# Optimization experiments

Measured on AMD Instinct MI355X. Metric: run time of the kernel, lower is better.

The kernel has to match this reference:

```python
import jax, jax.numpy as jnp
import numpy as np

B, K, V = 8192, 1024, 2


def setup_inputs() -> dict:
    key = jax.random.key(0)
    k1, k2, k3, k4, k5, k6 = jax.random.split(key, 6)
    z = jax.random.normal(k1, (B, K), dtype=jnp.float32)
    # -1 means no intervention for that sample
    intervention_target = jax.random.randint(k2, (B,), -1, K)
    intervention_variant = jax.random.randint(k3, (B,), 0, V)
    raw_adjacency = jax.random.normal(k4, (K, K), dtype=jnp.float32) * 0.05
    intervention_means = jax.random.normal(k5, (K, V), dtype=jnp.float32)
    intervention_log_scales = jax.random.normal(k6, (K, V), dtype=jnp.float32) * 0.1
    return {
        "z": z,
        "intervention_target": intervention_target,
        "intervention_variant": intervention_variant,
        "raw_adjacency": raw_adjacency,
        "intervention_means": intervention_means,
        "intervention_log_scales": intervention_log_scales,
    }


def _scm_forward(z, target, variant, raw_adjacency, means, log_scales):
    Kd = z.shape[1]
    # strictly-lower-triangular adjacency (row j holds parents of node j)
    A = raw_adjacency * jnp.tril(jnp.ones((Kd, Kd), z.dtype), k=-1)

    def step(u, xs):
        a_row, mean_row, logsc_row, z_j, j = xs
        # forward substitution: u_j = z_j + sum_{i<j} A[j,i] * u_i
        # columns >= j of u are still zero and A row is zero there too
        value = z_j + u @ a_row  # [B]
        # intervention overwrite for samples with target == j
        m = mean_row[variant]                 # [B]
        s = jnp.exp(logsc_row[variant])       # [B]
        value = jnp.where(target == j, m + s * z_j, value)
        u = jax.lax.dynamic_update_slice(u, value[:, None], (0, j))
        return u, None

    u0 = jnp.zeros_like(z)
    xs = (A, means, log_scales, z.T, jnp.arange(Kd))
    u, _ = jax.lax.scan(step, u0, xs)
    return u


def reference(z, intervention_target, intervention_variant, raw_adjacency,
              intervention_means, intervention_log_scales):
    return _scm_forward(z, intervention_target, intervention_variant,
                        raw_adjacency, intervention_means, intervention_log_scales)
```

## Files before the change

### kernel.cpp

```cpp
#include <hip/hip_runtime.h>
#include <hip/hip_bf16.h>
#include <cstdint>

#define KDIM 1024
#define BDIM 8192
#define VDIM 2
#define NBLK 16

#if defined(__has_builtin)
#if __has_builtin(__builtin_amdgcn_global_load_lds)
#define HAS_GLL 1
#endif
#endif
#ifndef HAS_GLL
#define HAS_GLL 0
#endif

typedef __attribute__((ext_vector_type(8))) short short8;
typedef __attribute__((ext_vector_type(4))) float f32x4;

__device__ inline unsigned short f2bf(float x) {
  unsigned u = __builtin_bit_cast(unsigned, x);
  u = (u + 0x7FFFu + ((u >> 16) & 1u)) >> 16;
  return (unsigned short)u;
}

__device__ inline float bf2f(unsigned short x) {
  return __builtin_bit_cast(float, (unsigned)x << 16);
}


#define STAGE_T(DST, SRC, ROW0, COL0, LD)                                   \
  {                                                                         \
    const float* _s = (SRC);                                                \
    _Pragma("unroll") for (int _p = 0; _p < 4; ++_p) {                      \
      const int _m = _p * 16 + rw;                                          \
      float4 _v = *(const float4*)(_s + (size_t)((ROW0) + _m) * (LD) +      \
                                   (COL0) + 4 * k4);                        \
      (DST)[4 * k4 + 0][_m] = _v.x;                                         \
      (DST)[4 * k4 + 1][_m] = _v.y;                                         \
      (DST)[4 * k4 + 2][_m] = _v.z;                                         \
      (DST)[4 * k4 + 3][_m] = _v.w;                                         \
    }                                                                       \
  }

#define STAGE_D(DST, SRC, ROW0, COL0, LD)                                   \
  {                                                                         \
    const float* _s = (SRC);                                                \
    _Pragma("unroll") for (int _p = 0; _p < 4; ++_p) {                      \
      const int _kk = _p * 16 + rw;                                         \
      *(float4*)&(DST)[_kk][4 * k4] =                                       \
          *(const float4*)(_s + (size_t)((ROW0) + _kk) * (LD) + (COL0) +    \
                           4 * k4);                                         \
    }                                                                       \
  }

#define ZERO_ACC                                                            \
  _Pragma("unroll") for (int _a = 0; _a < 4; ++_a)                          \
      _Pragma("unroll") for (int _b = 0; _b < 4; ++_b) acc[_a][_b] = 0.f;

__device__ __forceinline__ void mac64(const float (*Ls)[68],
                                      const float (*Rs)[68], int tm, int tn,
                                      float acc[4][4]) {
#pragma unroll 4
  for (int k = 0; k < 64; ++k) {
    const float4 av = *(const float4*)&Ls[k][4 * tm];
    const float4 bv = *(const float4*)&Rs[k][4 * tn];
    const float aa[4] = {av.x, av.y, av.z, av.w};
    const float bb4[4] = {bv.x, bv.y, bv.z, bv.w};
#pragma unroll
    for (int a = 0; a < 4; ++a)
#pragma unroll
      for (int b = 0; b < 4; ++b) acc[a][b] += aa[a] * bb4[b];
  }
}

#define STORE_MT(R0, C0)                                                    \
  _Pragma("unroll") for (int _a = 0; _a < 4; ++_a) {                        \
    *(float4*)(MT + (size_t)((R0) + 4 * tm + _a) * KDIM + (C0) + 4 * tn) =  \
        make_float4(acc[_a][0], acc[_a][1], acc[_a][2], acc[_a][3]);        \
  }

#define MBF_TILE(R0, C0, BUF)                                               \
  {                                                                         \
    __syncthreads();                                                        \
    _Pragma("unroll") for (int _a = 0; _a < 4; ++_a)                        \
        _Pragma("unroll") for (int _b = 0; _b < 4; ++_b)                    \
            (BUF)[4 * tm + _a][4 * tn + _b] = acc[_a][_b];                  \
    __syncthreads();                                                        \
    const int _tr = tid >> 4, _tc = tid & 15;                               \
    _Pragma("unroll") for (int _p = 0; _p < 4; ++_p) {                      \
      const int _il = _p * 16 + _tr;                                        \
      ushort4 _o;                                                           \
      _o.x = f2bf((BUF)[4 * _tc + 0][_il]);                                 \
      _o.y = f2bf((BUF)[4 * _tc + 1][_il]);                                 \
      _o.z = f2bf((BUF)[4 * _tc + 2][_il]);                                 \
      _o.w = f2bf((BUF)[4 * _tc + 3][_il]);                                 \
      *(ushort4*)(Mbf + (size_t)((C0) + _il) * KDIM + (R0) + 4 * _tc) = _o; \
    }                                                                       \
  }

__global__ __launch_bounds__(256) void comb01(const float* __restrict__ A,
                                              float* __restrict__ MT,
                                              unsigned short* __restrict__ Mbf) {
  int b = blockIdx.x;
  const int rt = b & 1;
  const int jt = (b >> 1) & 1;
  const int s = b >> 2;
  const int base = s * 256;

  __shared__ float shpool[6 * 64 * 68];
  float (*Ls)[68] = (float(*)[68])(shpool);
  float (*Rs)[68] = (float(*)[68])(shpool + 4352);
  float (*tQ0L)[68] = (float(*)[68])(shpool + 2 * 4352);
  float (*tQ0H)[68] = (float(*)[68])(shpool + 3 * 4352);
  float (*tP0)[68] = (float(*)[68])(shpool + 4 * 4352);
  float (*tP1)[68] = (float(*)[68])(shpool + 5 * 4352);

  const int tid = threadIdx.x;
  const int k4 = tid & 15;
  const int rw = tid >> 4;
  const int tm = tid >> 4;
  const int tn = tid & 15;
  float acc[4][4];

  {
    float* Tt = shpool;
    float* As4 = shpool + 2 * 4352;
    const int g = tid >> 6;
    const int l = tid & 63;
    const int dbase = base + g * 64;
    float* Asg = As4 + g * 4160;

    for (int r = 0; r < 64; ++r)
      Asg[r * 65 + l] = A[(size_t)(dbase + r) * KDIM + dbase + l];
    __syncthreads();

    {
      const int h = l >> 5, c = l & 31;
      const float* Ah = Asg + (32 * h) * 65 + 32 * h;
      float m[32];
#pragma unroll
      for (int r = 0; r < 32; ++r) m[r] = (r == c) ? 1.f : 0.f;
#pragma unroll
      for (int r = 1; r < 32; ++r) {
        float a0 = 0.f, a1 = 0.f;
#pragma unroll
        for (int i = 0; i < 32; ++i) {
          if (i >= r) break;
          if (i & 1) a1 += Ah[r * 65 + i] * m[i];
          else       a0 += Ah[r * 65 + i] * m[i];
        }
        const float v = a0 + a1;
        m[r] = (r > c) ? v : m[r];
      }
      float* Th = Tt + g * 2112 + h * 1056;
#pragma unroll
      for (int r = 0; r < 32; ++r) Th[r * 33 + c] = m[r];
    }
    __syncthreads();

    const int tm8 = l >> 3, tn8 = l & 7;
    {
      float u[4][4];
#pragma unroll
      for (int a = 0; a < 4; ++a)
#pragma unroll
        for (int b2 = 0; b2 < 4; ++b2) u[a][b2] = 0.f;
      const float* T1 = Tt + g * 2112;
#pragma unroll
      for (int ki = 0; ki < 8; ++ki) {
        float4 av[4], bv[4];
#pragma unroll
        for (int a = 0; a < 4; ++a)
          av[a] = *(const float4*)&Asg[(32 + 4 * tm8 + a) * 65 + 4 * ki];
#pragma unroll
        for (int j = 0; j < 4; ++j)
          bv[j] = *(const float4*)&T1[(4 * ki + j) * 33 + 4 * tn8];
#pragma unroll
        for (int a = 0; a < 4; ++a) {
          const float aa[4] = {av[a].x, av[a].y, av[a].z, av[a].w};
#pragma unroll
          for (int j = 0; j < 4; ++j) {
            const float bb[4] = {bv[j].x, bv[j].y, bv[j].z, bv[j].w};
#pragma unroll
            for (int b2 = 0; b2 < 4; ++b2) u[a][b2] += aa[j] * bb[b2];
          }
        }
      }
#pragma unroll
      for (int a = 0; a < 4; ++a)
#pragma unroll
        for (int b2 = 0; b2 < 4; ++b2)
          Asg[(4 * tm8 + a) * 32 + 4 * tn8 + b2] = u[a][b2];
    }
    __syncthreads();

    {
      float t21[4][4];
#pragma unroll
      for (int a = 0; a < 4; ++a)
#pragma unroll
        for (int b2 = 0; b2 < 4; ++b2) t21[a][b2] = 0.f;
      const float* T2 = Tt + g * 2112 + 1056;
#pragma unroll
      for (int ki = 0; ki < 8; ++ki) {
        float4 av[4], bv[4];
#pragma unroll
        for (int a = 0; a < 4; ++a)
          av[a] = *(const float4*)&T2[(4 * tm8 + a) * 33 + 4 * ki];
#pragma unroll
        for (int j = 0; j < 4; ++j)
          bv[j] = *(const float4*)&Asg[(4 * ki + j) * 32 + 4 * tn8];
#pragma unroll
        for (int a = 0; a < 4; ++a) {
          const float aa[4] = {av[a].x, av[a].y, av[a].z, av[a].w};
#pragma unroll
          for (int j = 0; j < 4; ++j) {
            const float bb[4] = {bv[j].x, bv[j].y, bv[j].z, bv[j].w};
#pragma unroll
            for (int b2 = 0; b2 < 4; ++b2) t21[a][b2] += aa[j] * bb[b2];
          }
        }
      }
#pragma unroll
      for (int a = 0; a < 4; ++a)
#pragma unroll
        for (int b2 = 0; b2 < 4; ++b2)
          Asg[1024 + (4 * tm8 + a) * 32 + 4 * tn8 + b2] = t21[a][b2];
    }
    __syncthreads();

    {
      const float* T21 = Asg + 1024;
      const float* Tg = Tt + g * 2112;
      for (int r4 = 0; r4 < 16; ++r4) {
        float vals[4];
#pragma unroll
        for (int j = 0; j < 4; ++j) {
          const int r = 4 * r4 + j;
          float v;
          if (r < 32)
            v = (l < 32) ? Tg[r * 33 + l] : 0.f;
          else
            v = (l < 32) ? T21[(r - 32) * 32 + l]
                         : Tg[1056 + (r - 32) * 33 + (l - 32)];
          vals[j] = v;
        }
        *(float4*)(MT + (size_t)(dbase + l) * KDIM + dbase + 4 * r4) =
            make_float4(vals[0], vals[1], vals[2], vals[3]);
      }
      if (jt == 0 && rt == 0) {
        for (int r = 0; r < 64; ++r) {
          float v;
          if (r < 32)
            v = (l < 32) ? Tg[r * 33 + l] : 0.f;
          else
            v = (l < 32) ? T21[(r - 32) * 32 + l]
                         : Tg[1056 + (r - 32) * 33 + (l - 32)];
          Mbf[(size_t)(dbase + r) * KDIM + dbase + l] = f2bf(v);
        }
      }
    }
    __syncthreads();
  }

  if (jt == 0) {
    STAGE_T(Ls, MT, base, base, KDIM);
    STAGE_T(Rs, A, base + 64, base, KDIM);
    __syncthreads();
    ZERO_ACC;
    mac64(Ls, Rs, tm, tn, acc);
    __syncthreads();
#pragma unroll
    for (int a = 0; a < 4; ++a)
#pragma unroll
      for (int b2 = 0; b2 < 4; ++b2) tP0[4 * tn + b2][4 * tm + a] = acc[a][b2];
    STAGE_D(Rs, MT, base + 64, base + 64, KDIM);
    __syncthreads();
    ZERO_ACC;
    mac64(tP0, Rs, tm, tn, acc);
    __syncthreads();
#pragma unroll
    for (int a = 0; a < 4; ++a)
#pragma unroll
      for (int b2 = 0; b2 < 4; ++b2) tQ0L[4 * tn + b2][4 * tm + a] = acc[a][b2];
    if (rt == 0) {
      STORE_MT(base, base + 64);
      MBF_TILE(base, base + 64, Rs);
    }
  }
  __syncthreads();

  if (rt == 1) {
    STAGE_T(Ls, MT, base + 128, base + 128, KDIM);
    STAGE_T(Rs, A, base + 192, base + 128, KDIM);
    __syncthreads();
    ZERO_ACC;
    mac64(Ls, Rs, tm, tn, acc);
    __syncthreads();
#pragma unroll
    for (int a = 0; a < 4; ++a)
#pragma unroll
      for (int b2 = 0; b2 < 4; ++b2) tP1[4 * tn + b2][4 * tm + a] = acc[a][b2];
    STAGE_D(Rs, MT, base + 192, base + 192, KDIM);
    __syncthreads();
    ZERO_ACC;
    mac64(tP1, Rs, tm, tn, acc);
    __syncthreads();
#pragma unroll
    for (int a = 0; a < 4; ++a)
#pragma unroll
      for (int b2 = 0; b2 < 4; ++b2) tQ0H[4 * tm + a][4 * tn + b2] = acc[a][b2];
    if (jt == 1) {
      STORE_MT(base + 128, base + 192);
      MBF_TILE(base + 128, base + 192, Rs);
    }
  }
  __syncthreads();

  STAGE_T(Ls, MT, base + 64 * jt, base + 64 * jt, KDIM);
  __syncthreads();
  for (int kb2 = 0; kb2 <= rt; ++kb2) {
    ZERO_ACC;
    for (int kb = jt; kb < 2; ++kb) {
      STAGE_T(Rs, A, base + 128 + 64 * kb2, base + 64 * kb, KDIM);
      __syncthreads();
      mac64(kb == jt ? Ls : tQ0L, Rs, tm, tn, acc);
      __syncthreads();
    }
    if (kb2 == 0) {
#pragma unroll
      for (int a = 0; a < 4; ++a)
#pragma unroll
        for (int b2 = 0; b2 < 4; ++b2) tP0[4 * tn + b2][4 * tm + a] = acc[a][b2];
    } else {
#pragma unroll
      for (int a = 0; a < 4; ++a)
#pragma unroll
        for (int b2 = 0; b2 < 4; ++b2) tP1[4 * tn + b2][4 * tm + a] = acc[a][b2];
    }
  }
  __syncthreads();

  ZERO_ACC;
  if (rt == 0) {
    STAGE_D(Rs, MT, base + 128, base + 128, KDIM);
    __syncthreads();
    mac64(tP0, Rs, tm, tn, acc);
    __syncthreads();
  } else {
    mac64(tP0, tQ0H, tm, tn, acc);
    __syncthreads();
    STAGE_D(Rs, MT, base + 192, base + 192, KDIM);
    __syncthreads();
    mac64(tP1, Rs, tm, tn, acc);
    __syncthreads();
  }
  STORE_MT(base + 64 * jt, base + 128 + 64 * rt);
  MBF_TILE(base + 64 * jt, base + 128 + 64 * rt, Rs);
}

__global__ __launch_bounds__(256) void p4_stream(
    const float* __restrict__ A, float* __restrict__ MT,
    float* __restrict__ Pt, const float* __restrict__ Z,
    unsigned short* __restrict__ Zbf, unsigned short* __restrict__ Mbf,
    int do_zbf) {
  __shared__ float Ls[64][68];
  __shared__ float Rs[64][68];

  if (blockIdx.x >= 32) {
    const int wid = blockIdx.x - 32;
    const int nw = gridDim.x - 32;
    const int idx0 = wid * 256 + threadIdx.x;
    const int stride = nw * 256;
    const float4 z4 = make_float4(0.f, 0.f, 0.f, 0.f);
    const uint4 u4 = make_uint4(0u, 0u, 0u, 0u);

    for (int i = idx0; i < 256 * 1024; i += stride) {
      const int blk = i >> 10, off = i & 1023;
      const int bi = blk >> 4, bj = blk & 15;
      if (bi <= bj) continue;
      *(float4*)(MT + (size_t)(bi * 64 + (off >> 4)) * KDIM + bj * 64 +
                 4 * (off & 15)) = z4;
    }
    for (int i = idx0; i < 256 * 512; i += stride) {
      const int blk = i >> 9, off = i & 511;
      const int bi = blk >> 4, bj = blk & 15;
      if (bi >= bj) continue;
      *(uint4*)(Mbf + (size_t)(bi * 64 + (off >> 3)) * KDIM + bj * 64 +
                8 * (off & 7)) = u4;
    }
    if (do_zbf) {
      for (int i = idx0; i < BDIM * KDIM / 4; i += stride) {
        float4 v = *(const float4*)(Z + 4 * (size_t)i);
        ushort4 o;
        o.x = f2bf(v.x);
        o.y = f2bf(v.y);
        o.z = f2bf(v.z);
        o.w = f2bf(v.w);
        *(ushort4*)(Zbf + 4 * (size_t)i) = o;
      }
    }
    return;
  }

  int b = blockIdx.x;
  const int T = 4;
  const int rb = b % T; b /= T;
  const int jb = b % T; b /= T;
  const int c = b;
  const int h = 64 * T;
  const int base = c * 2 * h;

  const int tid = threadIdx.x;
  const int k4 = tid & 15;
  const int rw = tid >> 4;
  const int tm = tid >> 4;
  const int tn = tid & 15;
  float acc[4][4];
  ZERO_ACC;

  for (int kb = jb; kb < T; ++kb) {
    STAGE_T(Ls, MT, base + 64 * jb, base + 64 * kb, KDIM);
    STAGE_T(Rs, A, base + h + 64 * rb, base + 64 * kb, KDIM);
    __syncthreads();
    mac64(Ls, Rs, tm, tn, acc);
    __syncthreads();
  }

  float* P0 = Pt + (size_t)c * h * h;
#pragma unroll
  for (int a = 0; a < 4; ++a)
    *(float4*)(P0 + (size_t)(64 * jb + 4 * tm + a) * h + 64 * rb + 4 * tn) =
        make_float4(acc[a][0], acc[a][1], acc[a][2], acc[a][3]);
}

template <int T>
__global__ __launch_bounds__(256) void p_k(const float* __restrict__ A,
                                           const float* __restrict__ MT,
                                           float* __restrict__ Pt) {
  int b = blockIdx.x;
  const int rb = b % T; b /= T;
  const int jb = b % T; b /= T;
  const int c = b;
  const int h = 64 * T;
  const int base = c * 2 * h;

  __shared__ float Ls[64][68];
  __shared__ float Rs[64][68];
  const int tid = threadIdx.x;
  const int k4 = tid & 15;
  const int rw = tid >> 4;
  const int tm = tid >> 4;
  const int tn = tid & 15;
  float acc[4][4];
  ZERO_ACC;

  for (int kb = jb; kb < T; ++kb) {
    STAGE_T(Ls, MT, base + 64 * jb, base + 64 * kb, KDIM);
    STAGE_T(Rs, A, base + h + 64 * rb, base + 64 * kb, KDIM);
    __syncthreads();
    mac64(Ls, Rs, tm, tn, acc);
    __syncthreads();
  }

  float* P0 = Pt + (size_t)c * h * h;
#pragma unroll
  for (int a = 0; a < 4; ++a)
    *(float4*)(P0 + (size_t)(64 * jb + 4 * tm + a) * h + 64 * rb + 4 * tn) =
        make_float4(acc[a][0], acc[a][1], acc[a][2], acc[a][3]);
}

template <int T>
__global__ __launch_bounds__(256) void q_k(float* __restrict__ MT,
                                           const float* __restrict__ Pt,
                                           unsigned short* __restrict__ Mbf) {
  int b = blockIdx.x;
  const int rb = b % T; b /= T;
  const int jb = b % T; b /= T;
  const int c = b;
  const int h = 64 * T;
  const int base = c * 2 * h;

  __shared__ float Ls[64][68];
  __shared__ float Rs[64][68];
  const int tid = threadIdx.x;
  const int k4 = tid & 15;
  const int rw = tid >> 4;
  const int tm = tid >> 4;
  const int tn = tid & 15;
  float acc[4][4];
  ZERO_ACC;

  const float* P0 = Pt + (size_t)c * h * h;
  for (int kb = 0; kb <= rb; ++kb) {
    STAGE_T(Ls, P0, 64 * jb, 64 * kb, h);
    STAGE_D(Rs, MT, base + h + 64 * kb, base + h + 64 * rb, KDIM);
    __syncthreads();
    mac64(Ls, Rs, tm, tn, acc);
    __syncthreads();
  }

  STORE_MT(base + 64 * jb, base + h + 64 * rb);
  MBF_TILE(base + 64 * jb, base + h + 64 * rb, Ls);
}

#define LDB 72

template <int ZBF>
__global__ __launch_bounds__(256) void gemm_mfma(
    const float* __restrict__ Z, const unsigned short* __restrict__ Zbf,
    const unsigned short* __restrict__ Mbf, const float* __restrict__ MT,
    const int* __restrict__ tgt, const int* __restrict__ var,
    const float* __restrict__ means, const float* __restrict__ lsc,
    float* __restrict__ C) {
  __shared__ unsigned short As[128][LDB];
#if HAS_GLL
  __shared__ unsigned short Bs[128][64];
#else
  __shared__ unsigned short Bs[128][LDB];
#endif
  __shared__ float scoef[128];
  __shared__ int stb[128];

  const int d = blockIdx.x;
  const int xbl = d & 7;
  const int nir = (d >> 3) & 7;
  const int xbh = d >> 6;
  const int xb = xbh * 8 + xbl;
  const int ni = (xb & 32) ? (7 - nir) : nir;
  const int b0 = xb * 128;
  const int i0 = ni * 128;

  const int tid = threadIdx.x;
  const int w = tid >> 6;
  const int lane = tid & 63;
  const int wr = w >> 1, wc = w & 1;
  const int mlane = lane & 15;
  const int q = lane >> 4;

  const int rq = tid >> 4, kq = tid & 15;
  const int cb = tid >> 3, ck = tid & 7;

  f32x4 acc[4][4];
#pragma unroll
  for (int a = 0; a < 4; ++a)
#pragma unroll
    for (int b = 0; b < 4; ++b) acc[a][b] = (f32x4){0.f, 0.f, 0.f, 0.f};

  const int nkb = 2 * (ni + 1);
  for (int kb = 0; kb < nkb; ++kb) {
    const int k0 = kb * 64;
    if (ZBF) {
#pragma unroll
      for (int p = 0; p < 4; ++p) {
        const int r = p * 32 + cb;
        *(uint4*)&As[r][8 * ck] =
            *(const uint4*)(Zbf + (size_t)(b0 + r) * KDIM + k0 + 8 * ck);
      }
    } else {
#pragma unroll
      for (int p = 0; p < 8; ++p) {
        const int r = p * 16 + rq;
        float4 zv = *(const float4*)(Z + (size_t)(b0 + r) * KDIM + k0 + 4 * kq);
        ushort4 o;
        o.x = f2bf(zv.x);
        o.y = f2bf(zv.y);
        o.z = f2bf(zv.z);
        o.w = f2bf(zv.w);
        *(ushort4*)&As[r][4 * kq] = o;
      }
    }
#if HAS_GLL
    {
      const int rl = lane >> 3;
      const int ch = lane & 7;
#pragma unroll
      for (int i = 0; i < 4; ++i) {
        const int row = w * 32 + i * 8 + rl;
        const int sch = ch ^ (row & 7);
        const unsigned short* src =
            Mbf + (size_t)(i0 + row) * KDIM + k0 + sch * 8;
        __builtin_amdgcn_global_load_lds(
            (const __attribute__((address_space(1))) void*)src,
            (__attribute__((address_space(3))) void*)&Bs[w * 32 + i * 8][0],
            16, 0, 0);
      }
    }
#else
#pragma unroll
    for (int p = 0; p < 4; ++p) {
      const int c = p * 32 + cb;
      *(uint4*)&Bs[c][8 * ck] =
          *(const uint4*)(Mbf + (size_t)(i0 + c) * KDIM + k0 + 8 * ck);
    }
#endif
    __syncthreads();
#pragma unroll
    for (int ks = 0; ks < 2; ++ks) {
      const int kf = ks * 32 + q * 8;
      short8 av[4], bv[4];
#pragma unroll
      for (int a = 0; a < 4; ++a)
        av[a] = *(const short8*)&As[wr * 64 + 16 * a + mlane][kf];
#if HAS_GLL
      const char* BsB = (const char*)&Bs[0][0];
#pragma unroll
      for (int b = 0; b < 4; ++b) {
        const int row = wc * 64 + 16 * b + mlane;
        bv[b] = *(const short8*)(BsB + row * 128 +
                                 ((2 * kf) ^ ((row & 7) << 4)));
      }
#else
#pragma unroll
      for (int b = 0; b < 4; ++b)
        bv[b] = *(const short8*)&Bs[wc * 64 + 16 * b + mlane][kf];
#endif
#pragma unroll
      for (int a = 0; a < 4; ++a)
#pragma unroll
        for (int b = 0; b < 4; ++b)
          acc[a][b] =
              __builtin_amdgcn_mfma_f32_16x16x32_bf16(av[a], bv[b], acc[a][b], 0, 0, 0);
    }
    __syncthreads();
  }

  {
    const int s = tid >> 1, h2 = tid & 1;
    const int br = b0 + s;
    const int tb = tgt[br];
    float part = 0.f;
    if (tb >= 0) {
      const int nk16 = (tb >> 4) + 1;
      if (ZBF) {
        const unsigned short* zr = Zbf + (size_t)br * KDIM;
        const unsigned short* mr = Mbf + (size_t)tb * KDIM;
        for (int c16 = h2; c16 < nk16; c16 += 2) {
          const uint4 za = *(const uint4*)(zr + c16 * 16);
          const uint4 zb2 = *(const uint4*)(zr + c16 * 16 + 8);
          const uint4 ma = *(const uint4*)(mr + c16 * 16);
          const uint4 mb2 = *(const uint4*)(mr + c16 * 16 + 8);
          const unsigned zw[8] = {za.x, za.y, za.z, za.w,
                                  zb2.x, zb2.y, zb2.z, zb2.w};
          const unsigned mw[8] = {ma.x, ma.y, ma.z, ma.w,
                                  mb2.x, mb2.y, mb2.z, mb2.w};
#pragma unroll
          for (int wv = 0; wv < 8; ++wv) {
            part += __builtin_bit_cast(float, zw[wv] << 16) *
                    __builtin_bit_cast(float, mw[wv] << 16);
            part += __builtin_bit_cast(float, zw[wv] & 0xFFFF0000u) *
                    __builtin_bit_cast(float, mw[wv] & 0xFFFF0000u);
          }
        }
      } else {
        const float* zr = Z + (size_t)br * KDIM;
        const unsigned short* mr = Mbf + (size_t)tb * KDIM;
        const int nk8 = (tb >> 3) + 1;
        for (int c8 = h2; c8 < nk8; c8 += 2) {
          const float4 z0 = *(const float4*)(zr + c8 * 8);
          const float4 z1 = *(const float4*)(zr + c8 * 8 + 4);
          const ushort4 m0 = *(const ushort4*)(mr + c8 * 8);
          const ushort4 m1 = *(const ushort4*)(mr + c8 * 8 + 4);
          part += z0.x * bf2f(m0.x) + z0.y * bf2f(m0.y) + z0.z * bf2f(m0.z) +
                  z0.w * bf2f(m0.w) + z1.x * bf2f(m1.x) + z1.y * bf2f(m1.y) +
                  z1.z * bf2f(m1.z) + z1.w * bf2f(m1.w);
        }
      }
    }
    part += __shfl_down(part, 1);
    if (h2 == 0) {
      float cf = 0.f;
      int tbs = 0;
      if (tb >= 0) {
        const int v = var[br];
        const float mval = means[tb * VDIM + v];
        const float sval = expf(lsc[tb * VDIM + v]);
        const float zv = Z[(size_t)br * KDIM + tb];
        cf = (mval + sval * zv) - part;
        tbs = tb;
      }
      scoef[s] = cf;
      stb[s] = tbs;
    }
  }
  __syncthreads();

#pragma unroll
  for (int a = 0; a < 4; ++a) {
    const int l0 = wr * 64 + 16 * a + q * 4;
    const int row0 = b0 + l0;
#pragma unroll
    for (int b = 0; b < 4; ++b) {
      const int col = i0 + wc * 64 + 16 * b + mlane;
      float* Cp = C + (size_t)row0 * KDIM + col;
#pragma unroll
      for (int j = 0; j < 4; ++j) {
        const float cf = scoef[l0 + j];
        const float corr = cf * MT[(size_t)stb[l0 + j] * KDIM + col];
        Cp[j * KDIM] = acc[a][b][j] + corr;
      }
    }
  }
}

extern "C" void kernel_launch(void* const* d_in, const int* in_sizes, int n_in,
                              void* d_out, int out_size, void* d_ws,
                              size_t ws_size, hipStream_t stream) {
  const float* z = (const float*)d_in[0];
  const int* tgt = (const int*)d_in[1];
  const int* var = (const int*)d_in[2];
  const float* A = (const float*)d_in[3];
  const float* means = (const float*)d_in[4];
  const float* lsc = (const float*)d_in[5];
  float* out = (float*)d_out;

  char* ws = (char*)d_ws;
  float* MT = (float*)ws;
  unsigned short* Mbf = (unsigned short*)(ws + (4u << 20));
  float* Pt2 = (float*)(ws + (6u << 20));
  float* Pt3 = (float*)(ws + (6u << 20) + (512u << 10));
  unsigned short* Zbf = (unsigned short*)(ws + (7u << 20) + (512u << 10));
  const int use_zbf =
      ws_size >= (7u << 20) + (512u << 10) + (size_t)BDIM * KDIM * 2 ? 1 : 0;

  hipLaunchKernelGGL(comb01, dim3(16), dim3(256), 0, stream, A, MT, Mbf);
  hipLaunchKernelGGL(p4_stream, dim3(512), dim3(256), 0, stream, A, MT, Pt2, z,
                     Zbf, Mbf, use_zbf);
  hipLaunchKernelGGL((q_k<4>), dim3(32), dim3(256), 0, stream, MT, Pt2, Mbf);
  hipLaunchKernelGGL((p_k<8>), dim3(64), dim3(256), 0, stream, A, MT, Pt3);
  hipLaunchKernelGGL((q_k<8>), dim3(64), dim3(256), 0, stream, MT, Pt3, Mbf);
  if (use_zbf)
    hipLaunchKernelGGL((gemm_mfma<1>), dim3((BDIM / 128) * (KDIM / 128)),
                       dim3(256), 0, stream, z, Zbf, Mbf, MT, tgt, var, means,
                       lsc, out);
  else
    hipLaunchKernelGGL((gemm_mfma<0>), dim3((BDIM / 128) * (KDIM / 128)),
                       dim3(256), 0, stream, z, Zbf, Mbf, MT, tgt, var, means,
                       lsc, out);
}
```

Measured before the change: 246.2 us.

## Move fill/convert work into comb01 and register-prefetch tiles in p_k/q_k

The zero-fill of MT/Mbf and the Z-to-bf16 conversion move from the p4_stream kernel into extra blocks of comb01, launched with 256 blocks. The T=4 P step now uses the generic p_k<4> kernel. p_k and q_k prefetch the next k-tile into registers while the current tile's MAC runs, which hides global load latency behind compute. The risk is extra register pressure, and the comb01 grid now mixes the 16 critical-path blocks with a large bandwidth-bound conversion that may slow them.

```diff
diff --git a/kernel.cpp b/kernel.cpp
--- a/kernel.cpp
+++ b/kernel.cpp
@@ -53,6 +53,27 @@
           *(const float4*)(_s + (size_t)((ROW0) + _kk) * (LD) + (COL0) +    \
                            4 * k4);                                         \
     }                                                                       \
+  }
+
+#define LOADR(REG, SRC, ROW0, COL0, LD)                                     \
+  _Pragma("unroll") for (int _p = 0; _p < 4; ++_p) {                        \
+    (REG)[_p] = *(const float4*)((SRC) +                                    \
+                                 (size_t)((ROW0) + _p * 16 + rw) * (LD) +   \
+                                 (COL0) + 4 * k4);                          \
+  }
+
+#define WRT_T(DST, REG)                                                     \
+  _Pragma("unroll") for (int _p = 0; _p < 4; ++_p) {                        \
+    const int _m = _p * 16 + rw;                                            \
+    (DST)[4 * k4 + 0][_m] = (REG)[_p].x;                                    \
+    (DST)[4 * k4 + 1][_m] = (REG)[_p].y;                                    \
+    (DST)[4 * k4 + 2][_m] = (REG)[_p].z;                                    \
+    (DST)[4 * k4 + 3][_m] = (REG)[_p].w;                                    \
+  }
+
+#define WRT_D(DST, REG)                                                     \
+  _Pragma("unroll") for (int _p = 0; _p < 4; ++_p) {                        \
+    *(float4*)&(DST)[_p * 16 + rw][4 * k4] = (REG)[_p];                     \
   }
 
 #define ZERO_ACC                                                            \
@@ -102,7 +123,46 @@
 
 __global__ __launch_bounds__(256) void comb01(const float* __restrict__ A,
                                               float* __restrict__ MT,
-                                              unsigned short* __restrict__ Mbf) {
+                                              unsigned short* __restrict__ Mbf,
+                                              const float* __restrict__ Z,
+                                              unsigned short* __restrict__ Zbf,
+                                              int do_zbf) {
+  if (blockIdx.x >= NBLK) {
+    const int wid = blockIdx.x - NBLK;
+    const int nw = gridDim.x - NBLK;
+    const int idx0 = wid * 256 + threadIdx.x;
+    const int stride = nw * 256;
+    const float4 z4 = make_float4(0.f, 0.f, 0.f, 0.f);
+    const uint4 u4 = make_uint4(0u, 0u, 0u, 0u);
+
+    for (int i = idx0; i < 256 * 1024; i += stride) {
+      const int blk = i >> 10, off = i & 1023;
+      const int bi = blk >> 4, bj = blk & 15;
+      if (bi <= bj) continue;
+      *(float4*)(MT + (size_t)(bi * 64 + (off >> 4)) * KDIM + bj * 64 +
+                 4 * (off & 15)) = z4;
+    }
+    for (int i = idx0; i < 256 * 512; i += stride) {
+      const int blk = i >> 9, off = i & 511;
+      const int bi = blk >> 4, bj = blk & 15;
+      if (bi >= bj) continue;
+      *(uint4*)(Mbf + (size_t)(bi * 64 + (off >> 3)) * KDIM + bj * 64 +
+                8 * (off & 7)) = u4;
+    }
+    if (do_zbf) {
+      for (int i = idx0; i < BDIM * KDIM / 4; i += stride) {
+        float4 v = *(const float4*)(Z + 4 * (size_t)i);
+        ushort4 o;
+        o.x = f2bf(v.x);
+        o.y = f2bf(v.y);
+        o.z = f2bf(v.z);
+        o.w = f2bf(v.w);
+        *(ushort4*)(Zbf + 4 * (size_t)i) = o;
+      }
+    }
+    return;
+  }
+
   int b = blockIdx.x;
   const int rt = b & 1;
   const int jt = (b >> 1) & 1;
@@ -361,81 +421,6 @@
   MBF_TILE(base + 64 * jt, base + 128 + 64 * rt, Rs);
 }
 
-__global__ __launch_bounds__(256) void p4_stream(
-    const float* __restrict__ A, float* __restrict__ MT,
-    float* __restrict__ Pt, const float* __restrict__ Z,
-    unsigned short* __restrict__ Zbf, unsigned short* __restrict__ Mbf,
-    int do_zbf) {
-  __shared__ float Ls[64][68];
-  __shared__ float Rs[64][68];
-
-  if (blockIdx.x >= 32) {
-    const int wid = blockIdx.x - 32;
-    const int nw = gridDim.x - 32;
-    const int idx0 = wid * 256 + threadIdx.x;
-    const int stride = nw * 256;
-    const float4 z4 = make_float4(0.f, 0.f, 0.f, 0.f);
-    const uint4 u4 = make_uint4(0u, 0u, 0u, 0u);
-
-    for (int i = idx0; i < 256 * 1024; i += stride) {
-      const int blk = i >> 10, off = i & 1023;
-      const int bi = blk >> 4, bj = blk & 15;
-      if (bi <= bj) continue;
-      *(float4*)(MT + (size_t)(bi * 64 + (off >> 4)) * KDIM + bj * 64 +
-                 4 * (off & 15)) = z4;
-    }
-    for (int i = idx0; i < 256 * 512; i += stride) {
-      const int blk = i >> 9, off = i & 511;
-      const int bi = blk >> 4, bj = blk & 15;
-      if (bi >= bj) continue;
-      *(uint4*)(Mbf + (size_t)(bi * 64 + (off >> 3)) * KDIM + bj * 64 +
-                8 * (off & 7)) = u4;
-    }
-    if (do_zbf) {
-      for (int i = idx0; i < BDIM * KDIM / 4; i += stride) {
-        float4 v = *(const float4*)(Z + 4 * (size_t)i);
-        ushort4 o;
-        o.x = f2bf(v.x);
-        o.y = f2bf(v.y);
-        o.z = f2bf(v.z);
-        o.w = f2bf(v.w);
-        *(ushort4*)(Zbf + 4 * (size_t)i) = o;
-      }
-    }
-    return;
-  }
-
-  int b = blockIdx.x;
-  const int T = 4;
-  const int rb = b % T; b /= T;
-  const int jb = b % T; b /= T;
-  const int c = b;
-  const int h = 64 * T;
-  const int base = c * 2 * h;
-
-  const int tid = threadIdx.x;
-  const int k4 = tid & 15;
-  const int rw = tid >> 4;
-  const int tm = tid >> 4;
-  const int tn = tid & 15;
-  float acc[4][4];
-  ZERO_ACC;
-
-  for (int kb = jb; kb < T; ++kb) {
-    STAGE_T(Ls, MT, base + 64 * jb, base + 64 * kb, KDIM);
-    STAGE_T(Rs, A, base + h + 64 * rb, base + 64 * kb, KDIM);
-    __syncthreads();
-    mac64(Ls, Rs, tm, tn, acc);
-    __syncthreads();
-  }
-
-  float* P0 = Pt + (size_t)c * h * h;
-#pragma unroll
-  for (int a = 0; a < 4; ++a)
-    *(float4*)(P0 + (size_t)(64 * jb + 4 * tm + a) * h + 64 * rb + 4 * tn) =
-        make_float4(acc[a][0], acc[a][1], acc[a][2], acc[a][3]);
-}
-
 template <int T>
 __global__ __launch_bounds__(256) void p_k(const float* __restrict__ A,
                                            const float* __restrict__ MT,
@@ -457,10 +442,17 @@
   float acc[4][4];
   ZERO_ACC;
 
+  float4 lr[4], rr[4];
+  LOADR(lr, MT, base + 64 * jb, base + 64 * jb, KDIM);
+  LOADR(rr, A, base + h + 64 * rb, base + 64 * jb, KDIM);
   for (int kb = jb; kb < T; ++kb) {
-    STAGE_T(Ls, MT, base + 64 * jb, base + 64 * kb, KDIM);
-    STAGE_T(Rs, A, base + h + 64 * rb, base + 64 * kb, KDIM);
-    __syncthreads();
+    WRT_T(Ls, lr);
+    WRT_T(Rs, rr);
+    __syncthreads();
+    if (kb + 1 < T) {
+      LOADR(lr, MT, base + 64 * jb, base + 64 * (kb + 1), KDIM);
+      LOADR(rr, A, base + h + 64 * rb, base + 64 * (kb + 1), KDIM);
+    }
     mac64(Ls, Rs, tm, tn, acc);
     __syncthreads();
   }
@@ -494,10 +486,17 @@
   ZERO_ACC;
 
   const float* P0 = Pt + (size_t)c * h * h;
+  float4 lr[4], rr[4];
+  LOADR(lr, P0, 64 * jb, 0, h);
+  LOADR(rr, MT, base + h, base + h + 64 * rb, KDIM);
   for (int kb = 0; kb <= rb; ++kb) {
-    STAGE_T(Ls, P0, 64 * jb, 64 * kb, h);
-    STAGE_D(Rs, MT, base + h + 64 * kb, base + h + 64 * rb, KDIM);
-    __syncthreads();
+    WRT_T(Ls, lr);
+    WRT_D(Rs, rr);
+    __syncthreads();
+    if (kb + 1 <= rb) {
+      LOADR(lr, P0, 64 * jb, 64 * (kb + 1), h);
+      LOADR(rr, MT, base + h + 64 * (kb + 1), base + h + 64 * rb, KDIM);
+    }
     mac64(Ls, Rs, tm, tn, acc);
     __syncthreads();
   }
@@ -725,9 +724,9 @@
   const int use_zbf =
       ws_size >= (7u << 20) + (512u << 10) + (size_t)BDIM * KDIM * 2 ? 1 : 0;
 
-  hipLaunchKernelGGL(comb01, dim3(16), dim3(256), 0, stream, A, MT, Mbf);
-  hipLaunchKernelGGL(p4_stream, dim3(512), dim3(256), 0, stream, A, MT, Pt2, z,
-                     Zbf, Mbf, use_zbf);
+  hipLaunchKernelGGL(comb01, dim3(256), dim3(256), 0, stream, A, MT, Mbf, z,
+                     Zbf, use_zbf);
+  hipLaunchKernelGGL((p_k<4>), dim3(32), dim3(256), 0, stream, A, MT, Pt2);
   hipLaunchKernelGGL((q_k<4>), dim3(32), dim3(256), 0, stream, MT, Pt2, Mbf);
   hipLaunchKernelGGL((p_k<8>), dim3(64), dim3(256), 0, stream, A, MT, Pt3);
   hipLaunchKernelGGL((q_k<8>), dim3(64), dim3(256), 0, stream, MT, Pt3, Mbf);
```

Measured after the change: 248.5 us. Within noise of the previous version (+0.9%).
